# Optimization experiments

Measured on AMD Instinct MI355X. Metric: run time of the kernel, lower is better.

## Reference

```python
import jax, jax.numpy as jnp
import numpy as np

B, S, T = 1024, 1024, 16


def setup_inputs() -> dict:
    key = jax.random.key(0)
    k1, k2, k3, k4, k5 = jax.random.split(key, 5)
    emissions = jax.random.normal(k1, (B, S, T), dtype=jnp.float32)
    tags = jax.random.randint(k2, (B, S), 0, T, dtype=jnp.int64)
    mask = jnp.ones((B, S), dtype=bool)
    # parameters (original uses uniform(-0.1, 0.1) init)
    transitions = jax.random.uniform(k3, (T, T), minval=-0.1, maxval=0.1, dtype=jnp.float32)
    start_transitions = jax.random.uniform(k4, (T,), minval=-0.1, maxval=0.1, dtype=jnp.float32)
    end_transitions = jax.random.uniform(k5, (T,), minval=-0.1, maxval=0.1, dtype=jnp.float32)
    return {
        "emissions": emissions,
        "tags": tags,
        "mask": mask,
        "transitions": transitions,
        "start_transitions": start_transitions,
        "end_transitions": end_transitions,
    }


def _forward_algorithm(emissions, mask, transitions, start_transitions, end_transitions):
    # emissions: [B,S,T], mask: [B,S] bool -> log partition [B]
    score0 = start_transitions + emissions[:, 0]  # [B,T]

    def step(score, xs):
        em_t, m_t = xs  # em_t: [B,T], m_t: [B]
        # next[b,i,j] = score[b,i] + transitions[i,j] + em_t[b,j]
        nxt = score[:, :, None] + transitions[None, :, :] + em_t[:, None, :]
        nxt = jax.nn.logsumexp(nxt, axis=1)  # over previous tag i
        score = jnp.where(m_t[:, None], nxt, score)
        return score, None

    em_rest = jnp.swapaxes(emissions[:, 1:], 0, 1)  # [S-1,B,T]
    m_rest = jnp.swapaxes(mask[:, 1:], 0, 1)        # [S-1,B]
    score, _ = jax.lax.scan(step, score0, (em_rest, m_rest))
    score = score + end_transitions
    return jax.nn.logsumexp(score, axis=1)


def _score_sentence(emissions, tags, mask, transitions, start_transitions, end_transitions):
    # gold-path score, vectorized over time. [B]
    bidx = jnp.arange(emissions.shape[0])
    score = start_transitions[tags[:, 0]] + emissions[:, 0][bidx, tags[:, 0]]
    # per-step emission scores [B,S]
    emit = jnp.take_along_axis(emissions, tags[:, :, None], axis=2)[:, :, 0]
    # NOTE: faithful to original: transitions[tags[t], tags[t-1]]
    trans = transitions[tags[:, 1:], tags[:, :-1]]  # [B,S-1]
    m = mask[:, 1:].astype(emissions.dtype)
    score = score + jnp.sum((emit[:, 1:] + trans) * m, axis=1)
    last_idx = jnp.sum(mask.astype(jnp.int32), axis=1) - 1  # [B]
    last_tags = jnp.take_along_axis(tags, last_idx[:, None].astype(tags.dtype), axis=1)[:, 0]
    score = score + end_transitions[last_tags]
    return score


def reference(emissions, tags, mask, transitions, start_transitions, end_transitions):
    emissions = emissions.astype(jnp.float32)
    gold = _score_sentence(emissions, tags, mask, transitions, start_transitions, end_transitions)
    logZ = _forward_algorithm(emissions, mask, transitions, start_transitions, end_transitions)
    nll = logZ - gold
    return jnp.mean(nll)
```

## Files before the change

### kernel.cpp

```cpp
#include <hip/hip_runtime.h>
#include <stdint.h>


#define BB 1024
#define SS 1024
#define TT 16
#define CC 16
#define LL 64
#define P1B (BB * CC / 4)

typedef float    f32x4 __attribute__((ext_vector_type(4)));
typedef float    f32x2 __attribute__((ext_vector_type(2)));
typedef short    s16x4 __attribute__((ext_vector_type(4)));
typedef uint32_t u32x2 __attribute__((ext_vector_type(2)));

__device__ __forceinline__ uint32_t pkt(float lo, float hi) {
    return __builtin_amdgcn_perm(__float_as_uint(hi), __float_as_uint(lo), 0x07060302u);
}
__device__ __forceinline__ s16x4 mk_frag(uint32_t lo, uint32_t hi) {
    u32x2 t; t.x = lo; t.y = hi;
    return __builtin_bit_cast(s16x4, t);
}

__global__ __launch_bounds__(256) void fused1_kernel(
        const float* __restrict__ em,
        const float* __restrict__ trans,
        const int*   __restrict__ tags,
        const float* __restrict__ startt,
        const float* __restrict__ endt,
        float* __restrict__ mats,
        int*   __restrict__ scales,
        float* __restrict__ gold)
{
    __shared__ float red[256];
    if (blockIdx.x < P1B) {
        const int wave = threadIdx.x >> 6;
        const int lane = threadIdx.x & 63;
        const int id   = blockIdx.x * 4 + wave;
        const int b    = id >> 4;
        const int c    = id & 15;
        const int q    = lane >> 4;
        const int m    = lane & 15;

        const float comp = 1.00390625f;
        f32x2 e01, e23;
        e01.x = __expf(trans[(4*q + 0) * TT + m]) * comp;
        e01.y = __expf(trans[(4*q + 1) * TT + m]) * comp;
        e23.x = __expf(trans[(4*q + 2) * TT + m]) * comp;
        e23.y = __expf(trans[(4*q + 3) * TT + m]) * comp;

        f32x4 d;
        d[0] = (4*q + 0 == m) ? 1.f : 0.f;
        d[1] = (4*q + 1 == m) ? 1.f : 0.f;
        d[2] = (4*q + 2 == m) ? 1.f : 0.f;
        d[3] = (4*q + 3 == m) ? 1.f : 0.f;
        const f32x4 zero = {0.f, 0.f, 0.f, 0.f};
        int sc = 0;

        const float* ep = em + (size_t)b * SS * TT + (size_t)(c * LL) * TT + lane;

#define STEP(xv) {                                                          \
        const s16x4 bfr = mk_frag(pkt(d[0], d[1]), pkt(d[2], d[3]));        \
        f32x2 xx; xx.x = (xv); xx.y = (xv);                                 \
        const f32x2 a01 = xx * e01;                                         \
        const f32x2 a23 = xx * e23;                                         \
        const s16x4 afr = mk_frag(pkt(a01.x, a01.y), pkt(a23.x, a23.y));    \
        d = __builtin_amdgcn_mfma_f32_16x16x16bf16_1k(afr, bfr, zero, 0, 0, 0); }

#define SUB4(exv, P0) { _Pragma("unroll")                                   \
        for (int p = (P0); p < 4; ++p) {                                    \
            const float xp = __shfl((exv), p * 16 + m, 64);                 \
            STEP(xp); } }

#define RESCALE() {                                                         \
        float mx = fmaxf(fmaxf(d[0], d[1]), fmaxf(d[2], d[3]));             \
        mx = fmaxf(mx, __shfl_xor(mx, 16, 64));                             \
        mx = fmaxf(mx, __shfl_xor(mx, 32, 64));                             \
        const int e_ = (int)(__float_as_uint(mx) >> 23) - 127;              \
        const float sf_ = __uint_as_float((uint32_t)(127 - e_) << 23);      \
        d[0] *= sf_; d[1] *= sf_; d[2] *= sf_; d[3] *= sf_;                 \
        sc += e_; }

#define BLK8(P0) {                                                          \
        const float x0_ = ep[0];                                            \
        const float x1_ = ep[64];                                           \
        ep += 128;                                                          \
        const float ex0_ = __expf(x0_);                                     \
        const float ex1_ = __expf(x1_);                                     \
        SUB4(ex0_, P0);                                                     \
        SUB4(ex1_, 0);                                                      \
        RESCALE(); }

        if (c == 0) { BLK8(1); }
        const int nb = (c == 0) ? 7 : 8;
        for (int bbk = 0; bbk < nb; ++bbk) { BLK8(0); }
#undef STEP
#undef SUB4
#undef RESCALE
#undef BLK8

        float* mp = mats + (size_t)id * 256;
        mp[(4*q + 0) * TT + m] = d[0];
        mp[(4*q + 1) * TT + m] = d[1];
        mp[(4*q + 2) * TT + m] = d[2];
        mp[(4*q + 3) * TT + m] = d[3];
        if (q == 0) scales[id * 16 + m] = sc;
    } else {
        const int b = blockIdx.x - P1B, tid = threadIdx.x;
        float local = 0.f;
        for (int t = tid; t < SS; t += 256) {
            const int tg = tags[b * SS + t];
            float v = em[(size_t)(b * SS + t) * TT + tg];
            if (t > 0) v += trans[tg * TT + tags[b * SS + t - 1]];
            else       v += startt[tg];
            if (t == SS - 1) v += endt[tg];
            local += v;
        }
        red[tid] = local; __syncthreads();
        for (int s = 128; s > 0; s >>= 1) { if (tid < s) red[tid] += red[tid + s]; __syncthreads(); }
        if (tid == 0) gold[b] = red[0];
    }
}

__global__ __launch_bounds__(64) void phase2_kernel(
        const float* __restrict__ em,
        const float* __restrict__ startt,
        const float* __restrict__ endt,
        const float* __restrict__ mats,
        const int*   __restrict__ scales,
        const float* __restrict__ gold,
        float* __restrict__ out)
{
    const int lane = threadIdx.x;
    const int g    = lane >> 4;
    const int m    = lane & 15;
    const int b    = blockIdx.x * 4 + g;
    const int base = lane & 48;

    const float s0 = startt[m] + em[(size_t)b * SS * TT + m];
    float mx = s0;
    #pragma unroll
    for (int s = 1; s < 16; s <<= 1) mx = fmaxf(mx, __shfl_xor(mx, s, 16));
    float u   = __expf(s0 - mx);
    float ell = mx;

    for (int c = 0; c < CC; ++c) {
        const int idc = b * CC + c;
        int scm = scales[idc * 16 + m];
        int smax = scm;
        #pragma unroll
        for (int s = 1; s < 16; s <<= 1) smax = max(smax, __shfl_xor(smax, s, 16));
        const float up = ldexpf(u, scm - smax);

        const float* row = mats + (size_t)idc * 256 + m * TT;
        const f32x4 r0 = *(const f32x4*)(row + 0);
        const f32x4 r1 = *(const f32x4*)(row + 4);
        const f32x4 r2 = *(const f32x4*)(row + 8);
        const f32x4 r3 = *(const f32x4*)(row + 12);
        float acc = 0.f;
        #pragma unroll
        for (int k = 0; k < 4; ++k) acc += r0[k] * __shfl(up, base + k,      64);
        #pragma unroll
        for (int k = 0; k < 4; ++k) acc += r1[k] * __shfl(up, base + 4 + k,  64);
        #pragma unroll
        for (int k = 0; k < 4; ++k) acc += r2[k] * __shfl(up, base + 8 + k,  64);
        #pragma unroll
        for (int k = 0; k < 4; ++k) acc += r3[k] * __shfl(up, base + 12 + k, 64);

        float m2 = acc;
        #pragma unroll
        for (int s = 1; s < 16; s <<= 1) m2 = fmaxf(m2, __shfl_xor(m2, s, 16));
        u = acc / m2;
        ell += __logf(m2) + (float)smax * 0.6931471805599453f;
    }

    float v = u * __expf(endt[m]);
    #pragma unroll
    for (int s = 1; s < 16; s <<= 1) v += __shfl_xor(v, s, 16);

    float contrib = (m == 0) ? (ell + __logf(v) - gold[b]) : 0.f;
    #pragma unroll
    for (int s = 1; s < 64; s <<= 1) contrib += __shfl_xor(contrib, s, 64);
    if (lane == 0) atomicAdd(out, contrib * (1.0f / BB));
}

extern "C" void kernel_launch(void* const* d_in, const int* in_sizes, int n_in,
                              void* d_out, int out_size, void* d_ws, size_t ws_size,
                              hipStream_t stream) {
    const float* em     = (const float*)d_in[0];
    const int*   tags   = (const int*)  d_in[1];
    const float* trans  = (const float*)d_in[3];
    const float* startt = (const float*)d_in[4];
    const float* endt   = (const float*)d_in[5];
    float* out = (float*)d_out;

    float* mats   = (float*)d_ws;
    int*   scales = (int*)((char*)d_ws + (size_t)BB * CC * 256 * 4);
    float* gold   = (float*)((char*)scales + (size_t)BB * CC * 16 * 4);

    hipMemsetAsync(out, 0, sizeof(float), stream);
    fused1_kernel<<<P1B + BB, 256, 0, stream>>>(em, trans, tags, startt, endt, mats, scales, gold);
    phase2_kernel<<<BB / 4, 64, 0, stream>>>(em, startt, endt, mats, scales, gold, out);
}
```

Measured before the change: 145.7 us.

## Combine chunk matrices with MFMA and batch emission broadcasts via bpermute

The second-phase kernel now multiplies the per-chunk 16x16 transfer matrices together with bf16 MFMA, using one wave per sequence. It then applies the start vector once at the end, replacing the per-chunk scalar matrix-vector products done with shuffles. In phase one, the eight emission broadcasts per block are issued up front as ds_bpermute calls instead of interleaved __shfl calls, so they can overlap the MFMA chain. The matrix-matrix combine rounds the accumulated state to bf16 at every chunk, which may cost precision compared with the fp32 vector path.

```diff
diff --git a/kernel.cpp b/kernel.cpp
--- a/kernel.cpp
+++ b/kernel.cpp
@@ -11,6 +11,7 @@
 
 typedef float    f32x4 __attribute__((ext_vector_type(4)));
 typedef float    f32x2 __attribute__((ext_vector_type(2)));
+typedef int      i32x4 __attribute__((ext_vector_type(4)));
 typedef short    s16x4 __attribute__((ext_vector_type(4)));
 typedef uint32_t u32x2 __attribute__((ext_vector_type(2)));
 
@@ -42,6 +43,11 @@
         const int q    = lane >> 4;
         const int m    = lane & 15;
 
+        const int bpa0 = (m +  0) << 2;
+        const int bpa1 = (m + 16) << 2;
+        const int bpa2 = (m + 32) << 2;
+        const int bpa3 = (m + 48) << 2;
+
         const float comp = 1.00390625f;
         f32x2 e01, e23;
         e01.x = __expf(trans[(4*q + 0) * TT + m]) * comp;
@@ -66,11 +72,6 @@
         const f32x2 a23 = xx * e23;                                         \
         const s16x4 afr = mk_frag(pkt(a01.x, a01.y), pkt(a23.x, a23.y));    \
         d = __builtin_amdgcn_mfma_f32_16x16x16bf16_1k(afr, bfr, zero, 0, 0, 0); }
-
-#define SUB4(exv, P0) { _Pragma("unroll")                                   \
-        for (int p = (P0); p < 4; ++p) {                                    \
-            const float xp = __shfl((exv), p * 16 + m, 64);                 \
-            STEP(xp); } }
 
 #define RESCALE() {                                                         \
         float mx = fmaxf(fmaxf(d[0], d[1]), fmaxf(d[2], d[3]));             \
@@ -85,17 +86,25 @@
         const float x0_ = ep[0];                                            \
         const float x1_ = ep[64];                                           \
         ep += 128;                                                          \
-        const float ex0_ = __expf(x0_);                                     \
-        const float ex1_ = __expf(x1_);                                     \
-        SUB4(ex0_, P0);                                                     \
-        SUB4(ex1_, 0);                                                      \
+        const int ei0 = __float_as_int(__expf(x0_));                        \
+        const int ei1 = __float_as_int(__expf(x1_));                        \
+        float xp[8];                                                        \
+        xp[0] = __int_as_float(__builtin_amdgcn_ds_bpermute(bpa0, ei0));    \
+        xp[1] = __int_as_float(__builtin_amdgcn_ds_bpermute(bpa1, ei0));    \
+        xp[2] = __int_as_float(__builtin_amdgcn_ds_bpermute(bpa2, ei0));    \
+        xp[3] = __int_as_float(__builtin_amdgcn_ds_bpermute(bpa3, ei0));    \
+        xp[4] = __int_as_float(__builtin_amdgcn_ds_bpermute(bpa0, ei1));    \
+        xp[5] = __int_as_float(__builtin_amdgcn_ds_bpermute(bpa1, ei1));    \
+        xp[6] = __int_as_float(__builtin_amdgcn_ds_bpermute(bpa2, ei1));    \
+        xp[7] = __int_as_float(__builtin_amdgcn_ds_bpermute(bpa3, ei1));    \
+        _Pragma("unroll")                                                   \
+        for (int i = (P0); i < 8; ++i) { STEP(xp[i]); }                     \
         RESCALE(); }
 
         if (c == 0) { BLK8(1); }
         const int nb = (c == 0) ? 7 : 8;
         for (int bbk = 0; bbk < nb; ++bbk) { BLK8(0); }
 #undef STEP
-#undef SUB4
 #undef RESCALE
 #undef BLK8
 
@@ -122,7 +131,7 @@
     }
 }
 
-__global__ __launch_bounds__(64) void phase2_kernel(
+__global__ __launch_bounds__(256) void combine_kernel(
         const float* __restrict__ em,
         const float* __restrict__ startt,
         const float* __restrict__ endt,
@@ -131,57 +140,77 @@
         const float* __restrict__ gold,
         float* __restrict__ out)
 {
-    const int lane = threadIdx.x;
-    const int g    = lane >> 4;
+    const int wave = threadIdx.x >> 6;
+    const int lane = threadIdx.x & 63;
+    const int b    = blockIdx.x * 4 + wave;
+    const int q    = lane >> 4;
     const int m    = lane & 15;
-    const int b    = blockIdx.x * 4 + g;
-    const int base = lane & 48;
+
+    const float* m0 = mats + (size_t)(b * CC) * 256;
+    f32x4 d;
+    d[0] = m0[(4*q + 0) * TT + m];
+    d[1] = m0[(4*q + 1) * TT + m];
+    d[2] = m0[(4*q + 2) * TT + m];
+    d[3] = m0[(4*q + 3) * TT + m];
+    int sig = scales[(b * CC) * 16 + m];
+    int gam = 0;
+    const f32x4 zero = {0.f, 0.f, 0.f, 0.f};
+
+    #pragma unroll 4
+    for (int c = 1; c < CC; ++c) {
+        const int idc = b * CC + c;
+        const f32x4 a = *(const f32x4*)(mats + (size_t)idc * 256 + m * TT + 4 * q);
+        const i32x4 s = *(const i32x4*)(scales + idc * 16 + 4 * q);
+        int sm = max(max(s.x, s.y), max(s.z, s.w));
+        sm = max(sm, __shfl_xor(sm, 16, 64));
+        sm = max(sm, __shfl_xor(sm, 32, 64));
+        const float r0 = ldexpf(d[0], s.x - sm);
+        const float r1 = ldexpf(d[1], s.y - sm);
+        const float r2 = ldexpf(d[2], s.z - sm);
+        const float r3 = ldexpf(d[3], s.w - sm);
+        const s16x4 bfr = mk_frag(pkt(r0, r1), pkt(r2, r3));
+        const s16x4 afr = mk_frag(pkt(a.x, a.y), pkt(a.z, a.w));
+        d = __builtin_amdgcn_mfma_f32_16x16x16bf16_1k(afr, bfr, zero, 0, 0, 0);
+        gam += sm;
+        float mx = fmaxf(fmaxf(d[0], d[1]), fmaxf(d[2], d[3]));
+        mx = fmaxf(mx, __shfl_xor(mx, 16, 64));
+        mx = fmaxf(mx, __shfl_xor(mx, 32, 64));
+        const int e = (int)(__float_as_uint(mx) >> 23) - 127;
+        const float sf = __uint_as_float((uint32_t)(127 - e) << 23);
+        d[0] *= sf; d[1] *= sf; d[2] *= sf; d[3] *= sf;
+        sig += e;
+    }
 
     const float s0 = startt[m] + em[(size_t)b * SS * TT + m];
-    float mx = s0;
+    float mx0 = s0;
     #pragma unroll
-    for (int s = 1; s < 16; s <<= 1) mx = fmaxf(mx, __shfl_xor(mx, s, 16));
-    float u   = __expf(s0 - mx);
-    float ell = mx;
-
-    for (int c = 0; c < CC; ++c) {
-        const int idc = b * CC + c;
-        int scm = scales[idc * 16 + m];
-        int smax = scm;
-        #pragma unroll
-        for (int s = 1; s < 16; s <<= 1) smax = max(smax, __shfl_xor(smax, s, 16));
-        const float up = ldexpf(u, scm - smax);
-
-        const float* row = mats + (size_t)idc * 256 + m * TT;
-        const f32x4 r0 = *(const f32x4*)(row + 0);
-        const f32x4 r1 = *(const f32x4*)(row + 4);
-        const f32x4 r2 = *(const f32x4*)(row + 8);
-        const f32x4 r3 = *(const f32x4*)(row + 12);
-        float acc = 0.f;
-        #pragma unroll
-        for (int k = 0; k < 4; ++k) acc += r0[k] * __shfl(up, base + k,      64);
-        #pragma unroll
-        for (int k = 0; k < 4; ++k) acc += r1[k] * __shfl(up, base + 4 + k,  64);
-        #pragma unroll
-        for (int k = 0; k < 4; ++k) acc += r2[k] * __shfl(up, base + 8 + k,  64);
-        #pragma unroll
-        for (int k = 0; k < 4; ++k) acc += r3[k] * __shfl(up, base + 12 + k, 64);
-
-        float m2 = acc;
-        #pragma unroll
-        for (int s = 1; s < 16; s <<= 1) m2 = fmaxf(m2, __shfl_xor(m2, s, 16));
-        u = acc / m2;
-        ell += __logf(m2) + (float)smax * 0.6931471805599453f;
-    }
-
-    float v = u * __expf(endt[m]);
+    for (int s = 1; s < 16; s <<= 1) mx0 = fmaxf(mx0, __shfl_xor(mx0, s, 64));
+    const float u0n = __expf(s0 - mx0);
+
+    int sigmax = sig;
     #pragma unroll
-    for (int s = 1; s < 16; s <<= 1) v += __shfl_xor(v, s, 16);
-
-    float contrib = (m == 0) ? (ell + __logf(v) - gold[b]) : 0.f;
+    for (int s = 1; s < 16; s <<= 1) sigmax = max(sigmax, __shfl_xor(sigmax, s, 64));
+    const float w = ldexpf(u0n, sig - sigmax);
+
+    f32x4 v;
+    v[0] = d[0] * w; v[1] = d[1] * w; v[2] = d[2] * w; v[3] = d[3] * w;
     #pragma unroll
-    for (int s = 1; s < 64; s <<= 1) contrib += __shfl_xor(contrib, s, 64);
-    if (lane == 0) atomicAdd(out, contrib * (1.0f / BB));
+    for (int s = 1; s < 16; s <<= 1) {
+        v[0] += __shfl_xor(v[0], s, 64);
+        v[1] += __shfl_xor(v[1], s, 64);
+        v[2] += __shfl_xor(v[2], s, 64);
+        v[3] += __shfl_xor(v[3], s, 64);
+    }
+    const f32x4 ee = *(const f32x4*)(endt + 4 * q);
+    float z = __expf(ee.x) * v[0] + __expf(ee.y) * v[1]
+            + __expf(ee.z) * v[2] + __expf(ee.w) * v[3];
+    z += __shfl_xor(z, 16, 64);
+    z += __shfl_xor(z, 32, 64);
+
+    if (lane == 0) {
+        const float logZ = mx0 + 0.69314718055994531f * (float)(gam + sigmax) + __logf(z);
+        atomicAdd(out, (logZ - gold[b]) * (1.0f / BB));
+    }
 }
 
 extern "C" void kernel_launch(void* const* d_in, const int* in_sizes, int n_in,
@@ -200,5 +229,5 @@
 
     hipMemsetAsync(out, 0, sizeof(float), stream);
     fused1_kernel<<<P1B + BB, 256, 0, stream>>>(em, trans, tags, startt, endt, mats, scales, gold);
-    phase2_kernel<<<BB / 4, 64, 0, stream>>>(em, startt, endt, mats, scales, gold, out);
-}
+    combine_kernel<<<BB / 4, 256, 0, stream>>>(em, startt, endt, mats, scales, gold, out);
+}
```

After: 142.5 us. 1.02x faster.
